# Kernel optimization log

Hardware: AMD Instinct MI355X
Metric: run time of the kernel (lower is better)

Reference implementation:

```python
import jax, jax.numpy as jnp
import numpy as np

SEQ = 4096
D_IN = 1024
D_QK = 1024
D_V = 1024


def setup_inputs() -> dict:
    key = jax.random.key(0)
    kx, kq, kk, kv = jax.random.split(key, 4)
    x = jax.random.normal(kx, (SEQ, D_IN), dtype=jnp.float32)
    Wq = jax.random.uniform(kq, (D_IN, D_QK), dtype=jnp.float32)
    Wk = jax.random.uniform(kk, (D_IN, D_QK), dtype=jnp.float32)
    Wv = jax.random.uniform(kv, (D_IN, D_V), dtype=jnp.float32)
    return {"x": x, "Wq": Wq, "Wk": Wk, "Wv": Wv}


def reference(x, Wq, Wk, Wv):
    d_qk = Wq.shape[1]
    q = x @ Wq            # [T, d_qk]
    k = x @ Wk            # [T, d_qk]
    v = x @ Wv            # [T, d_v]
    scores = q @ k.T      # [T, T]
    T = scores.shape[0]
    # causal mask: positions j > i are masked with -inf BEFORE scaling
    causal = jnp.tril(jnp.ones((T, T), dtype=bool))
    masked = jnp.where(causal, scores, -jnp.inf)
    attn = jax.nn.softmax(masked / jnp.sqrt(jnp.asarray(d_qk, dtype=scores.dtype)), axis=-1)
    return attn @ v       # [T, d_v]
```

## Files before the change

kernel.cpp:

```cpp
#include <hip/hip_runtime.h>
#include <hip/hip_bf16.h>
#include <stdint.h>
#include <stddef.h>

#define SEQ 4096
#define DIN 1024
#define DQK 1024
#define DV  1024

typedef __bf16 bf16;
typedef __bf16 bf16x4 __attribute__((ext_vector_type(4)));
typedef __bf16 bf16x8 __attribute__((ext_vector_type(8)));
typedef float  f32x4  __attribute__((ext_vector_type(4)));

__global__ __launch_bounds__(256) void split_f32(const float* __restrict__ in,
                                                 bf16* __restrict__ hi,
                                                 bf16* __restrict__ lo, int n4) {
  int i = blockIdx.x * 256 + threadIdx.x;
  if (i >= n4) return;
  const float4 v = ((const float4*)in)[i];
  float a[4] = {v.x, v.y, v.z, v.w};
  bf16x4 h, l;
#pragma unroll
  for (int t = 0; t < 4; ++t) {
    bf16 hh = (bf16)a[t];
    h[t] = hh;
    l[t] = (bf16)(a[t] - (float)hh);
  }
  ((bf16x4*)hi)[i] = h;
  ((bf16x4*)lo)[i] = l;
}

template <bool DO_SPLIT>
__global__ __launch_bounds__(256) void wtrans(const float* __restrict__ W,
                                              bf16* __restrict__ outH,
                                              bf16* __restrict__ outL) {
  __shared__ float t[32][33];
  const int bx = blockIdx.x & 31;
  const int by = blockIdx.x >> 5;
  const int tx = threadIdx.x & 31;
  const int ty = threadIdx.x >> 5;
#pragma unroll
  for (int r = 0; r < 32; r += 8)
    t[ty + r][tx] = W[(size_t)(by * 32 + ty + r) * DQK + bx * 32 + tx];
  __syncthreads();
#pragma unroll
  for (int r = 0; r < 32; r += 8) {
    float v = t[tx][ty + r];
    size_t o = (size_t)(bx * 32 + ty + r) * DIN + by * 32 + tx;
    bf16 h = (bf16)v;
    outH[o] = h;
    if (DO_SPLIT) outL[o] = (bf16)(v - (float)h);
  }
}

__device__ __forceinline__ void stage_tile(const bf16* __restrict__ g, int ld,
                                           int row0, int k0, bf16* lds,
                                           int wid, int lane) {
#pragma unroll
  for (int c = 0; c < 2; ++c) {
    const int q = wid * 2 + c;
    const bf16* src =
        g + (size_t)(row0 + q * 16 + (lane >> 2)) * ld + k0 + (lane & 3) * 8;
    __builtin_amdgcn_global_load_lds(
        (const __attribute__((address_space(1))) void*)src,
        (__attribute__((address_space(3))) void*)(lds + q * 512), 16, 0, 0);
  }
}

__device__ __forceinline__ bf16x8 ldsfrag(const bf16* s, int rbase, int lane) {
  return *(const bf16x8*)&s[(rbase + (lane & 15)) * 32 + ((lane >> 4) * 8)];
}

template <bool SPLIT>
__device__ __forceinline__ void proj_body(
    const bf16* __restrict__ Agh, const bf16* __restrict__ Agl,
    const bf16* __restrict__ Bgh, const bf16* __restrict__ Bgl,
    bf16* __restrict__ outH, bf16* __restrict__ outL, int bm, int bn, int ldo,
    bf16* sAh, bf16* sBh, bf16* sAl, bf16* sBl) {
  const int wid = threadIdx.x >> 6;
  const int lane = threadIdx.x & 63;
  const int wr = (wid >> 1) * 64;
  const int wc = (wid & 1) * 64;

  f32x4 acc[4][4];
#pragma unroll
  for (int i = 0; i < 4; ++i)
#pragma unroll
    for (int j = 0; j < 4; ++j) acc[i][j] = (f32x4)(0.0f);

  for (int kt = 0; kt < DIN / 32; ++kt) {
    const int k0 = kt * 32;
    __syncthreads();
    stage_tile(Agh, DIN, bm * 128, k0, sAh, wid, lane);
    stage_tile(Bgh, DIN, bn * 128, k0, sBh, wid, lane);
    if (SPLIT) {
      stage_tile(Agl, DIN, bm * 128, k0, sAl, wid, lane);
      stage_tile(Bgl, DIN, bn * 128, k0, sBl, wid, lane);
    }
    __syncthreads();

    bf16x8 ah[4], bh[4];
#pragma unroll
    for (int i = 0; i < 4; ++i) ah[i] = ldsfrag(sAh, wr + i * 16, lane);
#pragma unroll
    for (int j = 0; j < 4; ++j) bh[j] = ldsfrag(sBh, wc + j * 16, lane);
#pragma unroll
    for (int i = 0; i < 4; ++i)
#pragma unroll
      for (int j = 0; j < 4; ++j)
        acc[i][j] = __builtin_amdgcn_mfma_f32_16x16x32_bf16(ah[i], bh[j],
                                                            acc[i][j], 0, 0, 0);
    if (SPLIT) {
      bf16x8 bl[4];
#pragma unroll
      for (int j = 0; j < 4; ++j) bl[j] = ldsfrag(sBl, wc + j * 16, lane);
#pragma unroll
      for (int i = 0; i < 4; ++i)
#pragma unroll
        for (int j = 0; j < 4; ++j)
          acc[i][j] = __builtin_amdgcn_mfma_f32_16x16x32_bf16(
              ah[i], bl[j], acc[i][j], 0, 0, 0);
      bf16x8 al[4];
#pragma unroll
      for (int i = 0; i < 4; ++i) al[i] = ldsfrag(sAl, wr + i * 16, lane);
#pragma unroll
      for (int i = 0; i < 4; ++i)
#pragma unroll
        for (int j = 0; j < 4; ++j)
          acc[i][j] = __builtin_amdgcn_mfma_f32_16x16x32_bf16(
              al[i], bh[j], acc[i][j], 0, 0, 0);
    }
  }

  const int r0 = bm * 128 + wr + ((lane >> 4) * 4);
  const int c0 = bn * 128 + wc + (lane & 15);
#pragma unroll
  for (int i = 0; i < 4; ++i)
#pragma unroll
    for (int j = 0; j < 4; ++j)
#pragma unroll
      for (int r = 0; r < 4; ++r) {
        const size_t o = (size_t)(r0 + i * 16 + r) * ldo + (c0 + j * 16);
        const float v = acc[i][j][r];
        bf16 h = (bf16)v;
        outH[o] = h;
        if (SPLIT) outL[o] = (bf16)(v - (float)h);
      }
}

__global__ __launch_bounds__(256, 2) void fused_proj(
    const bf16* __restrict__ xh, const bf16* __restrict__ xl,
    const bf16* __restrict__ wqh, const bf16* __restrict__ wql,
    const bf16* __restrict__ wkh, const bf16* __restrict__ wkl,
    const bf16* __restrict__ wvt, bf16* __restrict__ qh, bf16* __restrict__ ql,
    bf16* __restrict__ kh, bf16* __restrict__ kl, bf16* __restrict__ vt) {
  __shared__ bf16 sAh[128 * 32];
  __shared__ bf16 sBh[128 * 32];
  __shared__ bf16 sAl[128 * 32];
  __shared__ bf16 sBl[128 * 32];
  const int b = blockIdx.x;
  if (b < 256) {
    proj_body<true>(xh, xl, wqh, wql, qh, ql, b >> 3, b & 7, DQK, sAh, sBh, sAl,
                    sBl);
  } else if (b < 512) {
    const int bb = b - 256;
    proj_body<true>(xh, xl, wkh, wkl, kh, kl, bb >> 3, bb & 7, DQK, sAh, sBh,
                    sAl, sBl);
  } else {
    const int bb = b - 512;
    proj_body<false>(wvt, nullptr, xh, nullptr, vt, nullptr, bb >> 5, bb & 31,
                     SEQ, sAh, sBh, sAl, sBl);
  }
}

__global__ __launch_bounds__(256, 2) void score1(const bf16* __restrict__ qh,
                                                 const bf16* __restrict__ kh,
                                                 float* __restrict__ S) {
  __shared__ bf16 sA[128 * 32];
  __shared__ bf16 sB[128 * 32];
  const int t = blockIdx.x;
  int bi = (int)((sqrtf(8.0f * (float)t + 1.0f) - 1.0f) * 0.5f);
  while ((bi + 1) * (bi + 2) / 2 <= t) ++bi;
  while (bi * (bi + 1) / 2 > t) --bi;
  const int bm = bi;
  const int bn = t - bi * (bi + 1) / 2;

  const int wid = threadIdx.x >> 6;
  const int lane = threadIdx.x & 63;
  const int wr = (wid >> 1) * 64;
  const int wc = (wid & 1) * 64;

  f32x4 acc[4][4];
#pragma unroll
  for (int i = 0; i < 4; ++i)
#pragma unroll
    for (int j = 0; j < 4; ++j) acc[i][j] = (f32x4)(0.0f);

  for (int kt = 0; kt < DQK / 32; ++kt) {
    const int k0 = kt * 32;
    __syncthreads();
    stage_tile(qh, DQK, bm * 128, k0, sA, wid, lane);
    stage_tile(kh, DQK, bn * 128, k0, sB, wid, lane);
    __syncthreads();
    bf16x8 a[4], b[4];
#pragma unroll
    for (int i = 0; i < 4; ++i) a[i] = ldsfrag(sA, wr + i * 16, lane);
#pragma unroll
    for (int j = 0; j < 4; ++j) b[j] = ldsfrag(sB, wc + j * 16, lane);
#pragma unroll
    for (int i = 0; i < 4; ++i)
#pragma unroll
      for (int j = 0; j < 4; ++j)
        acc[i][j] = __builtin_amdgcn_mfma_f32_16x16x32_bf16(a[i], b[j],
                                                            acc[i][j], 0, 0, 0);
  }

  const int r0 = bm * 128 + wr + ((lane >> 4) * 4);
  const int c0 = bn * 128 + wc + (lane & 15);
#pragma unroll
  for (int i = 0; i < 4; ++i)
#pragma unroll
    for (int j = 0; j < 4; ++j)
#pragma unroll
      for (int r = 0; r < 4; ++r)
        S[(size_t)(r0 + i * 16 + r) * SEQ + (c0 + j * 16)] = acc[i][j][r];
}

__global__ __launch_bounds__(256) void softmax_fixup(
    float* __restrict__ S, const bf16* __restrict__ qh,
    const bf16* __restrict__ ql, const bf16* __restrict__ kh,
    const bf16* __restrict__ kl) {
  __shared__ __align__(16) float rb[4][4096];
  const int wid = threadIdx.x >> 6;
  const int lane = threadIdx.x & 63;
  const int row = blockIdx.x * 4 + wid;
  const int len = row + 1;
  const int ext = ((row >> 7) + 1) << 7;
  float* srow = S + (size_t)row * SEQ;
  float* rbw = rb[wid];

  float m0 = -3.0e38f;
  for (int j = lane * 4; j < len; j += 256) {
    float4 v = *(const float4*)(srow + j);
    *(float4*)&rbw[j] = v;
    if (j + 0 < len) m0 = fmaxf(m0, v.x);
    if (j + 1 < len) m0 = fmaxf(m0, v.y);
    if (j + 2 < len) m0 = fmaxf(m0, v.z);
    if (j + 3 < len) m0 = fmaxf(m0, v.w);
  }
#pragma unroll
  for (int o = 32; o > 0; o >>= 1) m0 = fmaxf(m0, __shfl_xor(m0, o));
  __syncthreads();

  float q[16];
  {
    const size_t base = (size_t)row * DQK + lane * 16;
    bf16x8 h0 = *(const bf16x8*)(qh + base);
    bf16x8 h1 = *(const bf16x8*)(qh + base + 8);
    bf16x8 l0 = *(const bf16x8*)(ql + base);
    bf16x8 l1 = *(const bf16x8*)(ql + base + 8);
#pragma unroll
    for (int t = 0; t < 8; ++t) {
      q[t] = (float)h0[t] + (float)l0[t];
      q[8 + t] = (float)h1[t] + (float)l1[t];
    }
  }

  const float T = m0 - 1024.0f;
  float m = -3.0e38f;
  for (int base = 0; base < len; base += 64) {
    const int j = base + lane;
    const bool cand = (j < len) && (rbw[j] >= T);
    unsigned long long mask = __ballot(cand);
    while (mask) {
      const int jj = base + (int)__builtin_ctzll(mask);
      mask &= mask - 1;
      const size_t kb = (size_t)jj * DQK + lane * 16;
      bf16x8 h0 = *(const bf16x8*)(kh + kb);
      bf16x8 h1 = *(const bf16x8*)(kh + kb + 8);
      bf16x8 l0 = *(const bf16x8*)(kl + kb);
      bf16x8 l1 = *(const bf16x8*)(kl + kb + 8);
      float d = 0.f;
#pragma unroll
      for (int t = 0; t < 8; ++t) {
        d += q[t] * ((float)h0[t] + (float)l0[t]);
        d += q[8 + t] * ((float)h1[t] + (float)l1[t]);
      }
#pragma unroll
      for (int o = 32; o > 0; o >>= 1) d += __shfl_xor(d, o);
      if (lane == 0) rbw[jj] = d;
      m = fmaxf(m, d);
    }
  }
  __syncthreads();

  float lsum = 0.f;
  for (int j = lane * 4; j < len; j += 256) {
    float4 v = *(float4*)&rbw[j];
    float4 e;
    e.x = (j + 0 < len) ? __expf((v.x - m) * 0.03125f) : 0.f;
    e.y = (j + 1 < len) ? __expf((v.y - m) * 0.03125f) : 0.f;
    e.z = (j + 2 < len) ? __expf((v.z - m) * 0.03125f) : 0.f;
    e.w = (j + 3 < len) ? __expf((v.w - m) * 0.03125f) : 0.f;
    *(float4*)&rbw[j] = e;
    lsum += e.x + e.y + e.z + e.w;
  }
#pragma unroll
  for (int o = 32; o > 0; o >>= 1) lsum += __shfl_xor(lsum, o);
  const float inv = 1.0f / lsum;
  __syncthreads();

  bf16* prow = (bf16*)srow;
  for (int j = lane * 8; j < ext; j += 512) {
    bf16x8 o8;
#pragma unroll
    for (int t = 0; t < 8; ++t) {
      const int jj = j + t;
      const float v = (jj < len) ? rbw[jj] * inv : 0.f;
      o8[t] = (bf16)v;
    }
    *(bf16x8*)(prow + j) = o8;
  }
}

__global__ __launch_bounds__(256, 2) void pv_kernel(const bf16* __restrict__ P,
                                                    const bf16* __restrict__ vt,
                                                    float* __restrict__ out,
                                                    float* __restrict__ part) {
  __shared__ bf16 sA[128 * 32];
  __shared__ bf16 sB[128 * 32];
  const int g = blockIdx.x >> 3;
  const int bn = blockIdx.x & 7;
  int bm, slice;
  if (g < 8) {
    bm = g;
    slice = 0;
  } else if (g < 24) {
    const int i = g - 8;
    bm = 8 + (i >> 1);
    slice = i & 1;
  } else if (g < 48) {
    const int i = g - 24;
    bm = 16 + i / 3;
    slice = i % 3;
  } else {
    const int i = g - 48;
    bm = 24 + (i >> 2);
    slice = i & 3;
  }
  const int ks0 = slice * 32;
  const int kend = (bm + 1) * 4;
  const int nk = (ks0 + 32 < kend) ? ks0 + 32 : kend;

  const int wid = threadIdx.x >> 6;
  const int lane = threadIdx.x & 63;
  const int wr = (wid >> 1) * 64;
  const int wc = (wid & 1) * 64;

  f32x4 acc[4][4];
#pragma unroll
  for (int i = 0; i < 4; ++i)
#pragma unroll
    for (int j = 0; j < 4; ++j) acc[i][j] = (f32x4)(0.0f);

  for (int kt = ks0; kt < nk; ++kt) {
    const int k0 = kt * 32;
    __syncthreads();
    stage_tile(P, 2 * SEQ, bm * 128, k0, sA, wid, lane);
    stage_tile(vt, SEQ, bn * 128, k0, sB, wid, lane);
    __syncthreads();
    bf16x8 a[4], b[4];
#pragma unroll
    for (int i = 0; i < 4; ++i) a[i] = ldsfrag(sA, wr + i * 16, lane);
#pragma unroll
    for (int j = 0; j < 4; ++j) b[j] = ldsfrag(sB, wc + j * 16, lane);
#pragma unroll
    for (int i = 0; i < 4; ++i)
#pragma unroll
      for (int j = 0; j < 4; ++j)
        acc[i][j] = __builtin_amdgcn_mfma_f32_16x16x32_bf16(a[i], b[j],
                                                            acc[i][j], 0, 0, 0);
  }

  float* dst;
  int rbase;
  if (slice == 0) {
    dst = out;
    rbase = 0;
  } else if (slice == 1) {
    dst = part;
    rbase = 1024;
  } else if (slice == 2) {
    dst = part + 3145728;
    rbase = 2048;
  } else {
    dst = part + 5242880;
    rbase = 3072;
  }
  const int r0 = bm * 128 + wr + ((lane >> 4) * 4);
  const int c0 = bn * 128 + wc + (lane & 15);
#pragma unroll
  for (int i = 0; i < 4; ++i)
#pragma unroll
    for (int j = 0; j < 4; ++j)
#pragma unroll
      for (int r = 0; r < 4; ++r)
        dst[(size_t)(r0 + i * 16 + r - rbase) * DV + (c0 + j * 16)] =
            acc[i][j][r];
}

__global__ __launch_bounds__(256) void pv_reduce(const float* __restrict__ part,
                                                 float* __restrict__ out) {
  const int idx = blockIdx.x * 256 + threadIdx.x;
  const int r = 1024 + (idx >> 8);
  const int c4 = (idx & 255) * 4;
  const size_t o = (size_t)r * DV + c4;
  float4 acc = *(float4*)&out[o];
  const float4 p1 = *(const float4*)&part[(size_t)(r - 1024) * DV + c4];
  acc.x += p1.x; acc.y += p1.y; acc.z += p1.z; acc.w += p1.w;
  if (r >= 2048) {
    const float4 p2 =
        *(const float4*)&part[3145728 + (size_t)(r - 2048) * DV + c4];
    acc.x += p2.x; acc.y += p2.y; acc.z += p2.z; acc.w += p2.w;
  }
  if (r >= 3072) {
    const float4 p3 =
        *(const float4*)&part[5242880 + (size_t)(r - 3072) * DV + c4];
    acc.x += p3.x; acc.y += p3.y; acc.z += p3.z; acc.w += p3.w;
  }
  *(float4*)&out[o] = acc;
}

extern "C" void kernel_launch(void* const* d_in, const int* in_sizes, int n_in,
                              void* d_out, int out_size, void* d_ws,
                              size_t ws_size, hipStream_t stream) {
  const float* x = (const float*)d_in[0];
  const float* Wq = (const float*)d_in[1];
  const float* Wk = (const float*)d_in[2];
  const float* Wv = (const float*)d_in[3];
  float* out = (float*)d_out;
  char* ws = (char*)d_ws;

  const size_t MB = 1024 * 1024;
  const size_t OFF_QH = 0, OFF_QL = 8 * MB, OFF_KH = 16 * MB, OFF_KL = 24 * MB;
  const size_t OFF_PART = 0;
  const size_t OFF_VT = 32 * MB;
  const size_t OFF_S = 40 * MB;
  const size_t OFF_XH = 40 * MB, OFF_XL = 48 * MB;
  const size_t OFF_WQH = 56 * MB, OFF_WQL = 58 * MB;
  const size_t OFF_WKH = 60 * MB, OFF_WKL = 62 * MB, OFF_WVT = 64 * MB;
  const size_t NEEDED = 104 * MB;
  if (ws_size < NEEDED) return;

  bf16* qh = (bf16*)(ws + OFF_QH);
  bf16* ql = (bf16*)(ws + OFF_QL);
  bf16* kh = (bf16*)(ws + OFF_KH);
  bf16* kl = (bf16*)(ws + OFF_KL);
  float* part = (float*)(ws + OFF_PART);
  bf16* vt = (bf16*)(ws + OFF_VT);
  float* S = (float*)(ws + OFF_S);
  bf16* xh = (bf16*)(ws + OFF_XH);
  bf16* xl = (bf16*)(ws + OFF_XL);
  bf16* wqh = (bf16*)(ws + OFF_WQH);
  bf16* wql = (bf16*)(ws + OFF_WQL);
  bf16* wkh = (bf16*)(ws + OFF_WKH);
  bf16* wkl = (bf16*)(ws + OFF_WKL);
  bf16* wvt = (bf16*)(ws + OFF_WVT);

  split_f32<<<(SEQ * DIN / 4 + 255) / 256, 256, 0, stream>>>(x, xh, xl,
                                                             SEQ * DIN / 4);
  wtrans<true><<<1024, 256, 0, stream>>>(Wq, wqh, wql);
  wtrans<true><<<1024, 256, 0, stream>>>(Wk, wkh, wkl);
  wtrans<false><<<1024, 256, 0, stream>>>(Wv, wvt, nullptr);

  fused_proj<<<768, 256, 0, stream>>>(xh, xl, wqh, wql, wkh, wkl, wvt, qh, ql,
                                      kh, kl, vt);

  score1<<<(SEQ / 128) * (SEQ / 128 + 1) / 2, 256, 0, stream>>>(qh, kh, S);

  softmax_fixup<<<SEQ / 4, 256, 0, stream>>>(S, qh, ql, kh, kl);

  pv_kernel<<<640, 256, 0, stream>>>((const bf16*)S, vt, out, part);

  pv_reduce<<<(SEQ - 1024) * DV / 4 / 256, 256, 0, stream>>>(part, out);
}
```

Before: 189.6 us.

## Rewrite projection GEMM as pipelined 256x128 tiles and merge weight transposes

Replaces the fused projection kernel with a 512-thread kernel using 256x128 output tiles and a 4-deep LDS ring buffer. Global-to-LDS loads are issued two steps ahead under a single vmcnt wait and barrier per K step, instead of two syncthreads around each load. The split-precision passes (hi*hi, hi*lo, lo*hi) are flattened into one 96-step K loop so each step stages only one A/B pair. The three weight-transpose launches are merged into one kernel. This aims to hide load latency and cut launch and sync overhead, at the cost of fewer blocks (384) and more LDS per block.

```diff
diff --git a/kernel.cpp b/kernel.cpp
--- a/kernel.cpp
+++ b/kernel.cpp
@@ -31,13 +31,20 @@
   ((bf16x4*)lo)[i] = l;
 }
 
-template <bool DO_SPLIT>
-__global__ __launch_bounds__(256) void wtrans(const float* __restrict__ W,
-                                              bf16* __restrict__ outH,
-                                              bf16* __restrict__ outL) {
+__global__ __launch_bounds__(256) void wtrans_all(
+    const float* __restrict__ Wq, const float* __restrict__ Wk,
+    const float* __restrict__ Wv, bf16* __restrict__ wqh,
+    bf16* __restrict__ wql, bf16* __restrict__ wkh, bf16* __restrict__ wkl,
+    bf16* __restrict__ wvt) {
   __shared__ float t[32][33];
-  const int bx = blockIdx.x & 31;
-  const int by = blockIdx.x >> 5;
+  const int g = blockIdx.x >> 10;
+  const int bid = blockIdx.x & 1023;
+  const float* W = (g == 0) ? Wq : (g == 1) ? Wk : Wv;
+  bf16* outH = (g == 0) ? wqh : (g == 1) ? wkh : wvt;
+  bf16* outL = (g == 0) ? wql : wkl;
+  const bool do_split = (g < 2);
+  const int bx = bid & 31;
+  const int by = bid >> 5;
   const int tx = threadIdx.x & 31;
   const int ty = threadIdx.x >> 5;
 #pragma unroll
@@ -50,8 +57,142 @@
     size_t o = (size_t)(bx * 32 + ty + r) * DIN + by * 32 + tx;
     bf16 h = (bf16)v;
     outH[o] = h;
-    if (DO_SPLIT) outL[o] = (bf16)(v - (float)h);
-  }
+    if (do_split) outL[o] = (bf16)(v - (float)h);
+  }
+}
+
+__global__ __launch_bounds__(512, 2) void proj8(
+    const bf16* __restrict__ xh, const bf16* __restrict__ xl,
+    const bf16* __restrict__ wqh, const bf16* __restrict__ wql,
+    const bf16* __restrict__ wkh, const bf16* __restrict__ wkl,
+    const bf16* __restrict__ wvt, bf16* __restrict__ qh, bf16* __restrict__ ql,
+    bf16* __restrict__ kh, bf16* __restrict__ kl, bf16* __restrict__ vt) {
+  __shared__ bf16 lds[4 * 12288];
+  const int tid = threadIdx.x;
+  const int lane = tid & 63;
+  const int wid = tid >> 6;
+  const int wm = wid >> 1;
+  const int wn = wid & 1;
+  const int kq = lane >> 4;
+  const int r16 = lane & 15;
+
+  const int b = blockIdx.x;
+  const bf16 *Ah, *Al, *Bh, *Bl;
+  bf16 *oH, *oL;
+  int bm, bn, nt, ldo;
+  bool split;
+  if (b < 256) {
+    const bool isQ = b < 128;
+    const int bb = b & 127;
+    bm = bb >> 3;
+    bn = bb & 7;
+    nt = 96;
+    ldo = DQK;
+    split = true;
+    Ah = xh;
+    Al = xl;
+    Bh = isQ ? wqh : wkh;
+    Bl = isQ ? wql : wkl;
+    oH = isQ ? qh : kh;
+    oL = isQ ? ql : kl;
+  } else {
+    const int bb = b - 256;
+    bm = bb >> 5;
+    bn = bb & 31;
+    nt = 32;
+    ldo = SEQ;
+    split = false;
+    Ah = wvt;
+    Al = nullptr;
+    Bh = xh;
+    Bl = nullptr;
+    oH = vt;
+    oL = nullptr;
+  }
+  const int row0 = bm * 256, col0 = bn * 128;
+
+  auto STAGE = [&](int kt) {
+    const bf16* Ab = Ah;
+    const bf16* Bb = Bh;
+    int k0;
+    if (split) {
+      const int r = kt >> 5;
+      k0 = (kt & 31) * 32;
+      if (r == 2) Ab = Al;
+      if (r == 1) Bb = Bl;
+    } else {
+      k0 = kt * 32;
+    }
+    bf16* lb = lds + (kt & 3) * 12288;
+#pragma unroll
+    for (int l = 0; l < 2; ++l) {
+      const int c = l * 512 + tid;
+      const bf16* src =
+          Ab + (size_t)(row0 + (c & 255)) * DIN + k0 + (c >> 8) * 8;
+      __builtin_amdgcn_global_load_lds(
+          (const __attribute__((address_space(1))) void*)src,
+          (__attribute__((address_space(3))) void*)(lb + c * 8), 16, 0, 0);
+    }
+    {
+      const bf16* src =
+          Bb + (size_t)(col0 + (tid & 127)) * DIN + k0 + (tid >> 7) * 8;
+      __builtin_amdgcn_global_load_lds(
+          (const __attribute__((address_space(1))) void*)src,
+          (__attribute__((address_space(3))) void*)(lb + 8192 + tid * 8), 16, 0,
+          0);
+    }
+  };
+
+  f32x4 acc[4][4];
+#pragma unroll
+  for (int i = 0; i < 4; ++i)
+#pragma unroll
+    for (int j = 0; j < 4; ++j) acc[i][j] = (f32x4)(0.0f);
+
+  auto COMPUTE = [&](int kt) {
+    const bf16* lb = lds + (kt & 3) * 12288;
+    bf16x8 af[4], bfr[4];
+#pragma unroll
+    for (int f = 0; f < 4; ++f)
+      af[f] = *(const bf16x8*)(lb + kq * 2048 + (wm * 64 + f * 16 + r16) * 8);
+#pragma unroll
+    for (int f = 0; f < 4; ++f)
+      bfr[f] = *(const bf16x8*)(lb + 8192 + kq * 1024 +
+                                (wn * 64 + f * 16 + r16) * 8);
+    __builtin_amdgcn_s_setprio(1);
+#pragma unroll
+    for (int i = 0; i < 4; ++i)
+#pragma unroll
+      for (int j = 0; j < 4; ++j)
+        acc[i][j] = __builtin_amdgcn_mfma_f32_16x16x32_bf16(af[i], bfr[j],
+                                                            acc[i][j], 0, 0, 0);
+    __builtin_amdgcn_s_setprio(0);
+  };
+
+  STAGE(0);
+  STAGE(1);
+  for (int t = 0; t < nt - 1; ++t) {
+    asm volatile("s_waitcnt vmcnt(3)\n\ts_barrier" ::: "memory");
+    if (t + 2 < nt) STAGE(t + 2);
+    COMPUTE(t);
+  }
+  asm volatile("s_waitcnt vmcnt(0)\n\ts_barrier" ::: "memory");
+  COMPUTE(nt - 1);
+
+  const int r0 = row0 + wm * 64 + ((lane >> 4) * 4);
+  const int c0 = col0 + wn * 64 + r16;
+#pragma unroll
+  for (int i = 0; i < 4; ++i)
+#pragma unroll
+    for (int j = 0; j < 4; ++j)
+#pragma unroll
+      for (int r = 0; r < 4; ++r) {
+        const size_t o = (size_t)(r0 + i * 16 + r) * ldo + (c0 + j * 16);
+        const float v = acc[i][j][r];
+        bf16 h = (bf16)v;
+        oH[o] = h;
+        if (split) oL[o] = (bf16)(v - (float)h);
+      }
 }
 
 __device__ __forceinline__ void stage_tile(const bf16* __restrict__ g, int ld,
@@ -70,108 +211,6 @@
 
 __device__ __forceinline__ bf16x8 ldsfrag(const bf16* s, int rbase, int lane) {
   return *(const bf16x8*)&s[(rbase + (lane & 15)) * 32 + ((lane >> 4) * 8)];
-}
-
-template <bool SPLIT>
-__device__ __forceinline__ void proj_body(
-    const bf16* __restrict__ Agh, const bf16* __restrict__ Agl,
-    const bf16* __restrict__ Bgh, const bf16* __restrict__ Bgl,
-    bf16* __restrict__ outH, bf16* __restrict__ outL, int bm, int bn, int ldo,
-    bf16* sAh, bf16* sBh, bf16* sAl, bf16* sBl) {
-  const int wid = threadIdx.x >> 6;
-  const int lane = threadIdx.x & 63;
-  const int wr = (wid >> 1) * 64;
-  const int wc = (wid & 1) * 64;
-
-  f32x4 acc[4][4];
-#pragma unroll
-  for (int i = 0; i < 4; ++i)
-#pragma unroll
-    for (int j = 0; j < 4; ++j) acc[i][j] = (f32x4)(0.0f);
-
-  for (int kt = 0; kt < DIN / 32; ++kt) {
-    const int k0 = kt * 32;
-    __syncthreads();
-    stage_tile(Agh, DIN, bm * 128, k0, sAh, wid, lane);
-    stage_tile(Bgh, DIN, bn * 128, k0, sBh, wid, lane);
-    if (SPLIT) {
-      stage_tile(Agl, DIN, bm * 128, k0, sAl, wid, lane);
-      stage_tile(Bgl, DIN, bn * 128, k0, sBl, wid, lane);
-    }
-    __syncthreads();
-
-    bf16x8 ah[4], bh[4];
-#pragma unroll
-    for (int i = 0; i < 4; ++i) ah[i] = ldsfrag(sAh, wr + i * 16, lane);
-#pragma unroll
-    for (int j = 0; j < 4; ++j) bh[j] = ldsfrag(sBh, wc + j * 16, lane);
-#pragma unroll
-    for (int i = 0; i < 4; ++i)
-#pragma unroll
-      for (int j = 0; j < 4; ++j)
-        acc[i][j] = __builtin_amdgcn_mfma_f32_16x16x32_bf16(ah[i], bh[j],
-                                                            acc[i][j], 0, 0, 0);
-    if (SPLIT) {
-      bf16x8 bl[4];
-#pragma unroll
-      for (int j = 0; j < 4; ++j) bl[j] = ldsfrag(sBl, wc + j * 16, lane);
-#pragma unroll
-      for (int i = 0; i < 4; ++i)
-#pragma unroll
-        for (int j = 0; j < 4; ++j)
-          acc[i][j] = __builtin_amdgcn_mfma_f32_16x16x32_bf16(
-              ah[i], bl[j], acc[i][j], 0, 0, 0);
-      bf16x8 al[4];
-#pragma unroll
-      for (int i = 0; i < 4; ++i) al[i] = ldsfrag(sAl, wr + i * 16, lane);
-#pragma unroll
-      for (int i = 0; i < 4; ++i)
-#pragma unroll
-        for (int j = 0; j < 4; ++j)
-          acc[i][j] = __builtin_amdgcn_mfma_f32_16x16x32_bf16(
-              al[i], bh[j], acc[i][j], 0, 0, 0);
-    }
-  }
-
-  const int r0 = bm * 128 + wr + ((lane >> 4) * 4);
-  const int c0 = bn * 128 + wc + (lane & 15);
-#pragma unroll
-  for (int i = 0; i < 4; ++i)
-#pragma unroll
-    for (int j = 0; j < 4; ++j)
-#pragma unroll
-      for (int r = 0; r < 4; ++r) {
-        const size_t o = (size_t)(r0 + i * 16 + r) * ldo + (c0 + j * 16);
-        const float v = acc[i][j][r];
-        bf16 h = (bf16)v;
-        outH[o] = h;
-        if (SPLIT) outL[o] = (bf16)(v - (float)h);
-      }
-}
-
-__global__ __launch_bounds__(256, 2) void fused_proj(
-    const bf16* __restrict__ xh, const bf16* __restrict__ xl,
-    const bf16* __restrict__ wqh, const bf16* __restrict__ wql,
-    const bf16* __restrict__ wkh, const bf16* __restrict__ wkl,
-    const bf16* __restrict__ wvt, bf16* __restrict__ qh, bf16* __restrict__ ql,
-    bf16* __restrict__ kh, bf16* __restrict__ kl, bf16* __restrict__ vt) {
-  __shared__ bf16 sAh[128 * 32];
-  __shared__ bf16 sBh[128 * 32];
-  __shared__ bf16 sAl[128 * 32];
-  __shared__ bf16 sBl[128 * 32];
-  const int b = blockIdx.x;
-  if (b < 256) {
-    proj_body<true>(xh, xl, wqh, wql, qh, ql, b >> 3, b & 7, DQK, sAh, sBh, sAl,
-                    sBl);
-  } else if (b < 512) {
-    const int bb = b - 256;
-    proj_body<true>(xh, xl, wkh, wkl, kh, kl, bb >> 3, bb & 7, DQK, sAh, sBh,
-                    sAl, sBl);
-  } else {
-    const int bb = b - 512;
-    proj_body<false>(wvt, nullptr, xh, nullptr, vt, nullptr, bb >> 5, bb & 31,
-                     SEQ, sAh, sBh, sAl, sBl);
-  }
 }
 
 __global__ __launch_bounds__(256, 2) void score1(const bf16* __restrict__ qh,
@@ -470,12 +509,10 @@
 
   split_f32<<<(SEQ * DIN / 4 + 255) / 256, 256, 0, stream>>>(x, xh, xl,
                                                              SEQ * DIN / 4);
-  wtrans<true><<<1024, 256, 0, stream>>>(Wq, wqh, wql);
-  wtrans<true><<<1024, 256, 0, stream>>>(Wk, wkh, wkl);
-  wtrans<false><<<1024, 256, 0, stream>>>(Wv, wvt, nullptr);
-
-  fused_proj<<<768, 256, 0, stream>>>(xh, xl, wqh, wql, wkh, wkl, wvt, qh, ql,
-                                      kh, kl, vt);
+  wtrans_all<<<3072, 256, 0, stream>>>(Wq, Wk, Wv, wqh, wql, wkh, wkl, wvt);
+
+  proj8<<<384, 512, 0, stream>>>(xh, xl, wqh, wql, wkh, wkl, wvt, qh, ql, kh,
+                                 kl, vt);
 
   score1<<<(SEQ / 128) * (SEQ / 128 + 1) / 2, 256, 0, stream>>>(qh, kh, S);
 
```

Measured after the change: 258.6 us. 1.36x slower.
